# Performance work log

Hardware: AMD Instinct MI355X
Metric: run time of the kernel (lower is better)

## Reference

```python
import jax, jax.numpy as jnp
import numpy as np

B, D, T = 32, 6, 2048
FH, ENC, H, CONF, NC, K = 128, 128, 256, 64, 10, 5


def setup_inputs() -> dict:
    key = jax.random.key(0)
    ks = iter(jax.random.split(key, 40))
    n = lambda shape, s=0.05: jax.random.normal(next(ks), shape, dtype=jnp.float32) * s
    inp = {
        'M': jax.random.normal(next(ks), (B, D, T), dtype=jnp.float32),
        # causal conv frontend (4 dilated convs, kernel 5)
        'conv_w0': n((FH, D, K)), 'conv_b0': n((FH,)),
        'conv_w1': n((FH, FH, K)), 'conv_b1': n((FH,)),
        'conv_w2': n((FH, FH, K)), 'conv_b2': n((FH,)),
        'conv_w3': n((FH, FH, K)), 'conv_b3': n((FH,)),
        # encoder projection
        'enc_w': n((ENC, FH)), 'enc_b': n((ENC,)),
        # selective state space
        'A': n((H, H), 0.01), 'ip_w': n((H, ENC)), 'ip_b': n((H,)),
        'state_bias': jnp.zeros((H,), jnp.float32),
        'op_w': n((H, H)), 'op_b': n((H,)),
        # classifier head
        'cls_w1': n((256, H)), 'cls_b1': n((256,)),
        'cls_w2': n((NC, 256)), 'cls_b2': n((NC,)),
        # metanet: 2*D -> 64 -> 128 -> confound_dim
        'mn_w1': n((64, 2 * D)), 'mn_b1': n((64,)),
        'mn_w2': n((128, 64)), 'mn_b2': n((128,)),
        'mn_w3': n((CONF, 128)), 'mn_b3': n((CONF,)),
        # frontdoor: confound_dim -> 128 -> ssm_hidden
        'fd_w1': n((128, CONF)), 'fd_b1': n((128,)),
        'fd_w2': n((H, 128)), 'fd_b2': n((H,)),
    }
    return inp


def _causal_conv(x, w, b, d):
    # x: (B,C,T), w: (O,I,K). pad-left (K-1)*d == pad-both + trim-right in torch code
    y = jax.lax.conv_general_dilated(
        x, w, window_strides=(1,), padding=[((w.shape[2] - 1) * d, 0)],
        rhs_dilation=(d,), dimension_numbers=('NCH', 'OIH', 'NCH'))
    return jax.nn.relu(y + b[None, :, None])


def reference(M, conv_w0, conv_b0, conv_w1, conv_b1, conv_w2, conv_b2, conv_w3, conv_b3,
              enc_w, enc_b, A, ip_w, ip_b, state_bias, op_w, op_b,
              cls_w1, cls_b1, cls_w2, cls_b2,
              mn_w1, mn_b1, mn_w2, mn_b2, mn_w3, mn_b3,
              fd_w1, fd_b1, fd_w2, fd_b2):
    # frontend: 4 causal dilated convs with ReLU
    out = M
    for w, b, d in ((conv_w0, conv_b0, 1), (conv_w1, conv_b1, 2),
                    (conv_w2, conv_b2, 4), (conv_w3, conv_b3, 8)):
        out = _causal_conv(out, w, b, d)
    feat = jnp.einsum('bct,ec->bte', out, enc_w) + enc_b  # (B,T,ENC)
    # SSM: precompute input projection, then sequential scan over T
    u = jnp.einsum('bte,he->bth', feat, ip_w) + ip_b + state_bias  # (B,T,H)

    def step(h, ut):
        h = jax.nn.gelu(h @ A.T + ut, approximate=False)
        return h, h

    h0 = jnp.zeros((M.shape[0], A.shape[0]), M.dtype)
    _, hs = jax.lax.scan(step, h0, jnp.swapaxes(u, 0, 1))  # hs: (T,B,H)
    ssm_out = jnp.einsum('tbh,gh->btg', hs, op_w) + op_b  # (B,T,H)
    pooled = ssm_out.mean(axis=1)  # (B,H)
    logits = jax.nn.relu(pooled @ cls_w1.T + cls_b1) @ cls_w2.T + cls_b2
    # confounder summary: mean & unbiased std over time
    s = jnp.concatenate([M.mean(axis=2), jnp.std(M, axis=2, ddof=1)], axis=1)
    z = jax.nn.relu(s @ mn_w1.T + mn_b1)
    z = jax.nn.relu(z @ mn_w2.T + mn_b2)
    conf_hat = z @ mn_w3.T + mn_b3
    adj = jax.nn.relu(conf_hat @ fd_w1.T + fd_b1) @ fd_w2.T + fd_b2
    corrected = pooled - adj
    return (logits, pooled, corrected, conf_hat)
```

## Files before the change

kernel.cpp:

```cpp
#include <hip/hip_runtime.h>
#include <cmath>


typedef __bf16 bf16_t;
typedef bf16_t bf16x8 __attribute__((ext_vector_type(8)));
typedef bf16_t bf16x4 __attribute__((ext_vector_type(4)));
typedef float f32x4 __attribute__((ext_vector_type(4)));

__device__ __forceinline__ f32x4 mfma16(bf16x8 a, bf16x8 b, f32x4 c) {
  return __builtin_amdgcn_mfma_f32_16x16x32_bf16(a, b, c, 0, 0, 0);
}
__device__ __forceinline__ float gelu_fast(float x) {
  float x2 = x * x;
  float p = __builtin_fmaf(x2, -0.10295219f, -2.3022081278f);
  float e = __builtin_amdgcn_exp2f(x * p);
  return x * __builtin_amdgcn_rcpf(1.f + e);
}
__device__ __forceinline__ float bf2f(unsigned short us) {
  return __uint_as_float(((unsigned)us) << 16);
}

__global__ void k_repack(const float* __restrict__ w0, const float* __restrict__ w1,
                         const float* __restrict__ w2, const float* __restrict__ w3,
                         bf16_t* __restrict__ wb0, bf16_t* __restrict__ wb1,
                         bf16_t* __restrict__ wb2, bf16_t* __restrict__ wb3) {
  int idx = blockIdx.x * 256 + threadIdx.x;
  if (idx < 128 * 32) {
    int o = idx >> 5, k = idx & 31;
    float v = 0.f;
    if (k < 30) { int i = k / 5, kk = k - i * 5; v = w0[(o * 6 + i) * 5 + kk]; }
    wb0[idx] = (bf16_t)v;
    return;
  }
  int e = idx - 128 * 32;
  if (e < 3 * 5 * 128 * 128) {
    int layer = e / (5 * 128 * 128);
    int r = e - layer * (5 * 128 * 128);
    int ks = r / 16384;
    int o = (r >> 7) & 127;
    int i = r & 127;
    const float* w = layer == 0 ? w1 : layer == 1 ? w2 : w3;
    bf16_t* wb = layer == 0 ? wb1 : layer == 1 ? wb2 : wb3;
    wb[r] = (bf16_t)w[(o * 128 + i) * 5 + ks];
  }
}

__global__ void k_wce(const float* __restrict__ ip_w, const float* __restrict__ enc_w,
                      const float* __restrict__ enc_b, const float* __restrict__ ip_b,
                      const float* __restrict__ sbias, bf16_t* __restrict__ wce,
                      float* __restrict__ bce) {
  int h = blockIdx.x, c = threadIdx.x;
  float s = 0.f;
  for (int e = 0; e < 128; ++e) s += ip_w[h * 128 + e] * enc_w[e * 128 + c];
  wce[h * 128 + c] = (bf16_t)s;
  if (c == 0) {
    float bv = 0.f;
    for (int e = 0; e < 128; ++e) bv += ip_w[h * 128 + e] * enc_b[e];
    bce[h] = bv + ip_b[h] + sbias[h];
  }
}

__global__ __launch_bounds__(256) void k_conv0(const float* __restrict__ M,
                                               const bf16_t* __restrict__ wb0,
                                               const float* __restrict__ b0,
                                               bf16_t* __restrict__ out) {
  __shared__ float raw[6][136];
  __shared__ bf16_t Xe[128 * 40];
  const int tid = threadIdx.x;
  const int b = blockIdx.y, t0 = blockIdx.x * 128;
  for (int id = tid; id < 6 * 132; id += 256) {
    int i = id / 132, j = id - i * 132;
    int t = t0 - 4 + j;
    raw[i][j] = (t >= 0) ? M[((size_t)b * 6 + i) * 2048 + t] : 0.f;
  }
  __syncthreads();
  for (int id = tid; id < 128 * 32; id += 256) {
    int tl = id >> 5, k = id & 31;
    float v = 0.f;
    if (k < 30) { int i = k / 5, kk = k - i * 5; v = raw[i][tl + kk]; }
    Xe[tl * 40 + k] = (bf16_t)v;
  }
  __syncthreads();
  const int w = tid >> 6, lane = tid & 63, q = lane >> 4, l15 = lane & 15;
  const int k0 = q * 8;
  const f32x4 z4 = {0.f, 0.f, 0.f, 0.f};
  f32x4 acc[2][8];
#pragma unroll
  for (int mt = 0; mt < 2; ++mt)
#pragma unroll
    for (int nt = 0; nt < 8; ++nt) acc[mt][nt] = z4;
  bf16x8 af[2];
#pragma unroll
  for (int mt = 0; mt < 2; ++mt)
    af[mt] = *(const bf16x8*)&Xe[(w * 32 + mt * 16 + l15) * 40 + k0];
#pragma unroll
  for (int nt = 0; nt < 8; ++nt) {
    bf16x8 bf = *(const bf16x8*)&wb0[(nt * 16 + l15) * 32 + k0];
#pragma unroll
    for (int mt = 0; mt < 2; ++mt) acc[mt][nt] = mfma16(af[mt], bf, acc[mt][nt]);
  }
#pragma unroll
  for (int nt = 0; nt < 8; ++nt) {
    const int o = nt * 16 + l15;
    const float bias = b0[o];
#pragma unroll
    for (int mt = 0; mt < 2; ++mt) {
#pragma unroll
      for (int r = 0; r < 4; ++r) {
        int t = t0 + w * 32 + mt * 16 + q * 4 + r;
        float v = acc[mt][nt][r] + bias;
        out[((size_t)b * 2048 + t) * 128 + o] = (bf16_t)(v > 0.f ? v : 0.f);
      }
    }
  }
}

template <int DIL>
__global__ __launch_bounds__(256) void k_conv(const bf16_t* __restrict__ in,
                                              const bf16_t* __restrict__ wb,
                                              const float* __restrict__ bias,
                                              bf16_t* __restrict__ out) {
  __shared__ bf16_t Xs[160 * 136];
  const int tid = threadIdx.x;
  const int b = blockIdx.y, t0 = blockIdx.x * 128;
  const bf16_t* src = in + (size_t)b * 2048 * 128;
  for (int id = tid; id < 160 * 16; id += 256) {
    int r = id >> 4, ck = id & 15;
    int t = t0 + r - 32;
    int4 v = make_int4(0, 0, 0, 0);
    if (t >= 0) v = *(const int4*)(src + (size_t)t * 128 + ck * 8);
    *(int4*)&Xs[r * 136 + ck * 8] = v;
  }
  __syncthreads();
  const int w = tid >> 6, lane = tid & 63, q = lane >> 4, l15 = lane & 15;
  const f32x4 z4 = {0.f, 0.f, 0.f, 0.f};
  f32x4 acc[2][8];
#pragma unroll
  for (int mt = 0; mt < 2; ++mt)
#pragma unroll
    for (int nt = 0; nt < 8; ++nt) acc[mt][nt] = z4;
#pragma unroll
  for (int ks = 0; ks < 5; ++ks) {
    const int shift = (4 - ks) * DIL;
#pragma unroll
    for (int kt = 0; kt < 4; ++kt) {
      const int k0 = kt * 32 + q * 8;
      bf16x8 af[2];
#pragma unroll
      for (int mt = 0; mt < 2; ++mt)
        af[mt] = *(const bf16x8*)&Xs[(32 + w * 32 + mt * 16 + l15 - shift) * 136 + k0];
#pragma unroll
      for (int nt = 0; nt < 8; ++nt) {
        bf16x8 bf = *(const bf16x8*)&wb[((size_t)ks * 128 + nt * 16 + l15) * 128 + k0];
#pragma unroll
        for (int mt = 0; mt < 2; ++mt) acc[mt][nt] = mfma16(af[mt], bf, acc[mt][nt]);
      }
    }
  }
#pragma unroll
  for (int nt = 0; nt < 8; ++nt) {
    const int o = nt * 16 + l15;
    const float bv = bias[o];
#pragma unroll
    for (int mt = 0; mt < 2; ++mt) {
#pragma unroll
      for (int r = 0; r < 4; ++r) {
        int t = t0 + w * 32 + mt * 16 + q * 4 + r;
        float v = acc[mt][nt][r] + bv;
        out[((size_t)b * 2048 + t) * 128 + o] = (bf16_t)(v > 0.f ? v : 0.f);
      }
    }
  }
}

__global__ __launch_bounds__(256) void k_ugemm(const bf16_t* __restrict__ in,
                                               const bf16_t* __restrict__ wce,
                                               const float* __restrict__ bce,
                                               bf16_t* __restrict__ u) {
  __shared__ bf16_t Xs[128 * 136];
  const int tid = threadIdx.x;
  const int b = blockIdx.y, t0 = blockIdx.x * 128, hh = blockIdx.z;
  const bf16_t* src = in + (size_t)b * 2048 * 128;
  for (int id = tid; id < 128 * 16; id += 256) {
    int r = id >> 4, ck = id & 15;
    *(int4*)&Xs[r * 136 + ck * 8] = *(const int4*)(src + (size_t)(t0 + r) * 128 + ck * 8);
  }
  __syncthreads();
  const int w = tid >> 6, lane = tid & 63, q = lane >> 4, l15 = lane & 15;
  const f32x4 z4 = {0.f, 0.f, 0.f, 0.f};
  f32x4 acc[2][8];
#pragma unroll
  for (int mt = 0; mt < 2; ++mt)
#pragma unroll
    for (int nt = 0; nt < 8; ++nt) acc[mt][nt] = z4;
#pragma unroll
  for (int kt = 0; kt < 4; ++kt) {
    const int k0 = kt * 32 + q * 8;
    bf16x8 af[2];
#pragma unroll
    for (int mt = 0; mt < 2; ++mt)
      af[mt] = *(const bf16x8*)&Xs[(w * 32 + mt * 16 + l15) * 136 + k0];
#pragma unroll
    for (int nt = 0; nt < 8; ++nt) {
      bf16x8 bf = *(const bf16x8*)&wce[((size_t)hh * 128 + nt * 16 + l15) * 128 + k0];
#pragma unroll
      for (int mt = 0; mt < 2; ++mt) acc[mt][nt] = mfma16(af[mt], bf, acc[mt][nt]);
    }
  }
#pragma unroll
  for (int nt = 0; nt < 8; ++nt) {
    const int h = hh * 128 + nt * 16 + l15;
    const float bv = bce[h];
#pragma unroll
    for (int mt = 0; mt < 2; ++mt) {
#pragma unroll
      for (int r = 0; r < 4; ++r) {
        int t = t0 + w * 32 + mt * 16 + q * 4 + r;
        u[((size_t)b * 2048 + t) * 256 + h] = (bf16_t)(acc[mt][nt][r] + bv);
      }
    }
  }
}

__global__ __launch_bounds__(512, 2) void k_scan(const float* __restrict__ Am,
                                                 const bf16_t* __restrict__ u,
                                                 float* __restrict__ hbarOut) {
  __shared__ bf16_t Hs[2][16 * 256];
  const int b0 = blockIdx.x * 16;
  const int tid = threadIdx.x;
  const int wave = tid >> 6, lane = tid & 63, q = lane >> 4, l15 = lane & 15;

  bf16x8 afr[2][8];
#pragma unroll
  for (int ft = 0; ft < 2; ++ft) {
    const int f = wave * 32 + ft * 16 + l15;
#pragma unroll
    for (int kt = 0; kt < 8; ++kt) {
      const float* ap = Am + (size_t)f * 256 + kt * 32 + q * 8;
      f32x4 p0 = *(const f32x4*)ap;
      f32x4 p1 = *(const f32x4*)(ap + 4);
      bf16x8 v;
      v[0] = (bf16_t)p0[0]; v[1] = (bf16_t)p0[1]; v[2] = (bf16_t)p0[2]; v[3] = (bf16_t)p0[3];
      v[4] = (bf16_t)p1[0]; v[5] = (bf16_t)p1[1]; v[6] = (bf16_t)p1[2]; v[7] = (bf16_t)p1[3];
      afr[ft][kt] = v;
    }
  }
  for (int i = tid; i < 2 * 16 * 256 / 2; i += 512) ((int*)Hs)[i] = 0;

  const bf16_t* up = u + ((size_t)(b0 + l15) * 2048) * 256 + wave * 32 + q * 4;
  ushort4 uc[2], un[2];
#pragma unroll
  for (int ft = 0; ft < 2; ++ft) uc[ft] = *(const ushort4*)(up + ft * 16);
#pragma unroll
  for (int ft = 0; ft < 2; ++ft) un[ft] = *(const ushort4*)(up + 256 + ft * 16);

  float hbar[2][4];
#pragma unroll
  for (int ft = 0; ft < 2; ++ft)
#pragma unroll
    for (int r = 0; r < 4; ++r) hbar[ft][r] = 0.f;

  const int sw = l15 & 7;
  int rdoff[8];
#pragma unroll
  for (int kt = 0; kt < 8; ++kt) rdoff[kt] = l15 * 256 + (((kt * 4 + q) ^ sw) << 3);
  int wroff[2];
#pragma unroll
  for (int ft = 0; ft < 2; ++ft)
    wroff[ft] = l15 * 256 + (((wave * 4 + ft * 2 + (q >> 1)) ^ sw) << 3) + (q & 1) * 4;
  __syncthreads();

  int rd = 0;
  const f32x4 z4 = {0.f, 0.f, 0.f, 0.f};
#pragma unroll 2
  for (int t = 0; t < 2048; ++t) {
    bf16x8 hfr[8];
#pragma unroll
    for (int kt = 0; kt < 8; ++kt)
      hfr[kt] = *(const bf16x8*)&Hs[rd][rdoff[kt]];
    ushort4 u2[2];
    {
      size_t off = (size_t)(t + 2 <= 2047 ? t + 2 : 2047) * 256;
#pragma unroll
      for (int ft = 0; ft < 2; ++ft) u2[ft] = *(const ushort4*)(up + off + ft * 16);
    }
    f32x4 a0 = z4, a1 = z4;
#pragma unroll
    for (int kt = 0; kt < 8; ++kt) {
      a0 = mfma16(afr[0][kt], hfr[kt], a0);
      a1 = mfma16(afr[1][kt], hfr[kt], a1);
    }
    f32x4 acc01[2] = {a0, a1};
#pragma unroll
    for (int ft = 0; ft < 2; ++ft) {
      float g0 = gelu_fast(acc01[ft][0] + bf2f(uc[ft].x));
      float g1 = gelu_fast(acc01[ft][1] + bf2f(uc[ft].y));
      float g2 = gelu_fast(acc01[ft][2] + bf2f(uc[ft].z));
      float g3 = gelu_fast(acc01[ft][3] + bf2f(uc[ft].w));
      hbar[ft][0] += g0; hbar[ft][1] += g1; hbar[ft][2] += g2; hbar[ft][3] += g3;
      bf16x4 pk;
      pk[0] = (bf16_t)g0; pk[1] = (bf16_t)g1; pk[2] = (bf16_t)g2; pk[3] = (bf16_t)g3;
      *(bf16x4*)&Hs[rd ^ 1][wroff[ft]] = pk;
    }
    asm volatile("s_waitcnt lgkmcnt(0)\n\ts_barrier" ::: "memory");
#pragma unroll
    for (int ft = 0; ft < 2; ++ft) { uc[ft] = un[ft]; un[ft] = u2[ft]; }
    rd ^= 1;
  }
#pragma unroll
  for (int ft = 0; ft < 2; ++ft) {
    f32x4 vv;
#pragma unroll
    for (int r = 0; r < 4; ++r) vv[r] = hbar[ft][r] * (1.f / 2048.f);
    *(f32x4*)(hbarOut + (size_t)(b0 + l15) * 256 + wave * 32 + ft * 16 + q * 4) = vv;
  }
}

__global__ void k_meta1(const float* __restrict__ M, float* __restrict__ stats) {
  const int c = blockIdx.x, b = blockIdx.y, tid = threadIdx.x;
  const float* p = M + ((size_t)b * 6 + c) * 2048;
  float s = 0.f, ss = 0.f;
  for (int t = tid; t < 2048; t += 256) { float v = p[t]; s += v; ss += v * v; }
  for (int o = 32; o > 0; o >>= 1) { s += __shfl_down(s, o, 64); ss += __shfl_down(ss, o, 64); }
  __shared__ float as_[4], ass_[4];
  const int w = tid >> 6, lane = tid & 63;
  if (lane == 0) { as_[w] = s; ass_[w] = ss; }
  __syncthreads();
  if (tid == 0) {
    s = as_[0] + as_[1] + as_[2] + as_[3];
    ss = ass_[0] + ass_[1] + ass_[2] + ass_[3];
    float mean = s * (1.f / 2048.f);
    float var = (ss - 2048.f * mean * mean) * (1.f / 2047.f);
    if (var < 0.f) var = 0.f;
    stats[b * 12 + c] = mean;
    stats[b * 12 + 6 + c] = sqrtf(var);
  }
}

__global__ void k_meta2(const float* __restrict__ stats,
                        const float* __restrict__ w1, const float* __restrict__ b1,
                        const float* __restrict__ w2, const float* __restrict__ b2,
                        const float* __restrict__ w3, const float* __restrict__ b3,
                        const float* __restrict__ f1, const float* __restrict__ fb1,
                        const float* __restrict__ f2, const float* __restrict__ fb2,
                        float* __restrict__ out, float* __restrict__ adj) {
  const int b = blockIdx.x, tid = threadIdx.x;
  __shared__ float s[12], z1[64], z2[128], ch[64], a1[128];
  if (tid < 12) s[tid] = stats[b * 12 + tid];
  __syncthreads();
  if (tid < 64) {
    float v = b1[tid];
    for (int e = 0; e < 12; ++e) v += w1[tid * 12 + e] * s[e];
    z1[tid] = v > 0.f ? v : 0.f;
  }
  __syncthreads();
  if (tid < 128) {
    float v = b2[tid];
    for (int e = 0; e < 64; ++e) v += w2[tid * 64 + e] * z1[e];
    z2[tid] = v > 0.f ? v : 0.f;
  }
  __syncthreads();
  if (tid < 64) {
    float v = b3[tid];
    for (int e = 0; e < 128; ++e) v += w3[tid * 128 + e] * z2[e];
    ch[tid] = v;
    out[16704 + b * 64 + tid] = v;
  }
  __syncthreads();
  if (tid < 128) {
    float v = fb1[tid];
    for (int e = 0; e < 64; ++e) v += f1[tid * 64 + e] * ch[e];
    a1[tid] = v > 0.f ? v : 0.f;
  }
  __syncthreads();
  {
    float v = fb2[tid];
    for (int e = 0; e < 128; ++e) v += f2[tid * 128 + e] * a1[e];
    adj[b * 256 + tid] = v;
  }
}

__global__ void k_head(const float* __restrict__ hbar, const float* __restrict__ op_w,
                       const float* __restrict__ op_b, const float* __restrict__ cw1,
                       const float* __restrict__ cb1, const float* __restrict__ cw2,
                       const float* __restrict__ cb2, const float* __restrict__ adj,
                       float* __restrict__ out) {
  const int b = blockIdx.x, g = threadIdx.x;
  __shared__ float hs[256], ps[256], hid[256];
  hs[g] = hbar[b * 256 + g];
  __syncthreads();
  float v = op_b[g];
  for (int h = 0; h < 256; ++h) v += op_w[g * 256 + h] * hs[h];
  out[320 + b * 256 + g] = v;
  out[8512 + b * 256 + g] = v - adj[b * 256 + g];
  ps[g] = v;
  __syncthreads();
  float hv = cb1[g];
  for (int h = 0; h < 256; ++h) hv += cw1[g * 256 + h] * ps[h];
  hid[g] = hv > 0.f ? hv : 0.f;
  __syncthreads();
  if (g < 10) {
    float lv = cb2[g];
    for (int h = 0; h < 256; ++h) lv += cw2[g * 256 + h] * hid[h];
    out[b * 10 + g] = lv;
  }
}

extern "C" void kernel_launch(void* const* d_in, const int* in_sizes, int n_in,
                              void* d_out, int out_size, void* d_ws, size_t ws_size,
                              hipStream_t stream) {
  (void)in_sizes; (void)n_in; (void)out_size; (void)ws_size;
  const float* M    = (const float*)d_in[0];
  const float* w0   = (const float*)d_in[1];  const float* b0  = (const float*)d_in[2];
  const float* w1   = (const float*)d_in[3];  const float* b1  = (const float*)d_in[4];
  const float* w2   = (const float*)d_in[5];  const float* b2  = (const float*)d_in[6];
  const float* w3   = (const float*)d_in[7];  const float* b3  = (const float*)d_in[8];
  const float* encw = (const float*)d_in[9];  const float* encb = (const float*)d_in[10];
  const float* Am   = (const float*)d_in[11];
  const float* ipw  = (const float*)d_in[12]; const float* ipb = (const float*)d_in[13];
  const float* sb   = (const float*)d_in[14];
  const float* opw  = (const float*)d_in[15]; const float* opb = (const float*)d_in[16];
  const float* cw1  = (const float*)d_in[17]; const float* cb1 = (const float*)d_in[18];
  const float* cw2  = (const float*)d_in[19]; const float* cb2 = (const float*)d_in[20];
  const float* mw1  = (const float*)d_in[21]; const float* mb1 = (const float*)d_in[22];
  const float* mw2  = (const float*)d_in[23]; const float* mb2 = (const float*)d_in[24];
  const float* mw3  = (const float*)d_in[25]; const float* mb3 = (const float*)d_in[26];
  const float* fw1  = (const float*)d_in[27]; const float* fb1 = (const float*)d_in[28];
  const float* fw2  = (const float*)d_in[29]; const float* fb2 = (const float*)d_in[30];
  float* out = (float*)d_out;

  char* ws = (char*)d_ws;
  bf16_t* wb0  = (bf16_t*)(ws + 0);
  bf16_t* wb1  = (bf16_t*)(ws + 8192);
  bf16_t* wb2  = (bf16_t*)(ws + 172032);
  bf16_t* wb3  = (bf16_t*)(ws + 335872);
  bf16_t* wce  = (bf16_t*)(ws + 499712);
  float*  bce  = (float*) (ws + 565248);
  float*  hbar = (float*) (ws + 566272);
  float*  adj  = (float*) (ws + 599040);
  float*  stats= (float*) (ws + 631808);
  bf16_t* actA = (bf16_t*)(ws + 633856);
  bf16_t* actB = (bf16_t*)(ws + 17411072);
  bf16_t* u    = (bf16_t*)(ws + 34188288);

  k_repack<<<976, 256, 0, stream>>>(w0, w1, w2, w3, wb0, wb1, wb2, wb3);
  k_wce<<<256, 128, 0, stream>>>(ipw, encw, encb, ipb, sb, wce, bce);
  k_conv0<<<dim3(16, 32), 256, 0, stream>>>(M, wb0, b0, actA);
  k_conv<2><<<dim3(16, 32), 256, 0, stream>>>(actA, wb1, b1, actB);
  k_conv<4><<<dim3(16, 32), 256, 0, stream>>>(actB, wb2, b2, actA);
  k_conv<8><<<dim3(16, 32), 256, 0, stream>>>(actA, wb3, b3, actB);
  k_ugemm<<<dim3(16, 32, 2), 256, 0, stream>>>(actB, wce, bce, u);
  k_scan<<<2, 512, 0, stream>>>(Am, u, hbar);
  k_meta1<<<dim3(6, 32), 256, 0, stream>>>(M, stats);
  k_meta2<<<32, 256, 0, stream>>>(stats, mw1, mb1, mw2, mb2, mw3, mb3,
                                  fw1, fb1, fw2, fb2, out, adj);
  k_head<<<32, 256, 0, stream>>>(hbar, opw, opb, cw1, cb1, cw2, cb2, adj, out);
}
```

Before: 1.716 ms.

## Merge prep and meta kernels, restructure scan step with split MFMA chains

Folds the weight repack and encoder/input-projection precompute into one launch, and the metanet stats and MLP into one launch, cutting two kernel launches. The sequential scan loop is restructured. It manually unrolls by two with fixed LDS buffer offsets and splits the 8-deep MFMA accumulation into two independent chains. Odd waves iterate k-tiles in reverse order, and the hbar accumulation is deferred by one step to shorten the dependent path. The scan dominates runtime, so the latency-chain changes matter most. They cost more registers and add an extra vector add per step.

```diff
diff --git a/kernel.cpp b/kernel.cpp
--- a/kernel.cpp
+++ b/kernel.cpp
@@ -20,10 +20,27 @@
   return __uint_as_float(((unsigned)us) << 16);
 }
 
-__global__ void k_repack(const float* __restrict__ w0, const float* __restrict__ w1,
-                         const float* __restrict__ w2, const float* __restrict__ w3,
-                         bf16_t* __restrict__ wb0, bf16_t* __restrict__ wb1,
-                         bf16_t* __restrict__ wb2, bf16_t* __restrict__ wb3) {
+__global__ void k_prep(const float* __restrict__ w0, const float* __restrict__ w1,
+                       const float* __restrict__ w2, const float* __restrict__ w3,
+                       bf16_t* __restrict__ wb0, bf16_t* __restrict__ wb1,
+                       bf16_t* __restrict__ wb2, bf16_t* __restrict__ wb3,
+                       const float* __restrict__ ip_w, const float* __restrict__ enc_w,
+                       const float* __restrict__ enc_b, const float* __restrict__ ip_b,
+                       const float* __restrict__ sbias, bf16_t* __restrict__ wce,
+                       float* __restrict__ bce) {
+  if (blockIdx.x >= 976) {
+    const int hb = blockIdx.x - 976;
+    const int h = hb * 2 + (threadIdx.x >> 7), c = threadIdx.x & 127;
+    float s = 0.f;
+    for (int e = 0; e < 128; ++e) s += ip_w[h * 128 + e] * enc_w[e * 128 + c];
+    wce[h * 128 + c] = (bf16_t)s;
+    if (c == 0) {
+      float bv = 0.f;
+      for (int e = 0; e < 128; ++e) bv += ip_w[h * 128 + e] * enc_b[e];
+      bce[h] = bv + ip_b[h] + sbias[h];
+    }
+    return;
+  }
   int idx = blockIdx.x * 256 + threadIdx.x;
   if (idx < 128 * 32) {
     int o = idx >> 5, k = idx & 31;
@@ -42,21 +59,6 @@
     const float* w = layer == 0 ? w1 : layer == 1 ? w2 : w3;
     bf16_t* wb = layer == 0 ? wb1 : layer == 1 ? wb2 : wb3;
     wb[r] = (bf16_t)w[(o * 128 + i) * 5 + ks];
-  }
-}
-
-__global__ void k_wce(const float* __restrict__ ip_w, const float* __restrict__ enc_w,
-                      const float* __restrict__ enc_b, const float* __restrict__ ip_b,
-                      const float* __restrict__ sbias, bf16_t* __restrict__ wce,
-                      float* __restrict__ bce) {
-  int h = blockIdx.x, c = threadIdx.x;
-  float s = 0.f;
-  for (int e = 0; e < 128; ++e) s += ip_w[h * 128 + e] * enc_w[e * 128 + c];
-  wce[h * 128 + c] = (bf16_t)s;
-  if (c == 0) {
-    float bv = 0.f;
-    for (int e = 0; e < 128; ++e) bv += ip_w[h * 128 + e] * enc_b[e];
-    bce[h] = bv + ip_b[h] + sbias[h];
   }
 }
 
@@ -225,27 +227,39 @@
 __global__ __launch_bounds__(512, 2) void k_scan(const float* __restrict__ Am,
                                                  const bf16_t* __restrict__ u,
                                                  float* __restrict__ hbarOut) {
-  __shared__ bf16_t Hs[2][16 * 256];
+  __shared__ bf16_t HsF[2 * 16 * 256];
   const int b0 = blockIdx.x * 16;
   const int tid = threadIdx.x;
   const int wave = tid >> 6, lane = tid & 63, q = lane >> 4, l15 = lane & 15;
+  const int rev = wave & 1;
 
   bf16x8 afr[2][8];
-#pragma unroll
-  for (int ft = 0; ft < 2; ++ft) {
-    const int f = wave * 32 + ft * 16 + l15;
-#pragma unroll
-    for (int kt = 0; kt < 8; ++kt) {
+  int rdo0[8], rdo1[8];
+  const int sw = l15 & 7;
+#pragma unroll
+  for (int i = 0; i < 8; ++i) {
+    const int kt = rev ? 7 - i : i;
+#pragma unroll
+    for (int ft = 0; ft < 2; ++ft) {
+      const int f = wave * 32 + ft * 16 + l15;
       const float* ap = Am + (size_t)f * 256 + kt * 32 + q * 8;
       f32x4 p0 = *(const f32x4*)ap;
       f32x4 p1 = *(const f32x4*)(ap + 4);
       bf16x8 v;
       v[0] = (bf16_t)p0[0]; v[1] = (bf16_t)p0[1]; v[2] = (bf16_t)p0[2]; v[3] = (bf16_t)p0[3];
       v[4] = (bf16_t)p1[0]; v[5] = (bf16_t)p1[1]; v[6] = (bf16_t)p1[2]; v[7] = (bf16_t)p1[3];
-      afr[ft][kt] = v;
-    }
-  }
-  for (int i = tid; i < 2 * 16 * 256 / 2; i += 512) ((int*)Hs)[i] = 0;
+      afr[ft][i] = v;
+    }
+    rdo0[i] = l15 * 256 + (((kt * 4 + q) ^ sw) << 3);
+    rdo1[i] = 4096 + rdo0[i];
+  }
+  int wro0[2], wro1[2];
+#pragma unroll
+  for (int ft = 0; ft < 2; ++ft) {
+    wro0[ft] = l15 * 256 + (((wave * 4 + ft * 2 + (q >> 1)) ^ sw) << 3) + (q & 1) * 4;
+    wro1[ft] = 4096 + wro0[ft];
+  }
+  for (int i = tid; i < 2 * 16 * 256 / 2; i += 512) ((int*)HsF)[i] = 0;
 
   const bf16_t* up = u + ((size_t)(b0 + l15) * 2048) * 256 + wave * 32 + q * 4;
   ushort4 uc[2], un[2];
@@ -254,100 +268,106 @@
 #pragma unroll
   for (int ft = 0; ft < 2; ++ft) un[ft] = *(const ushort4*)(up + 256 + ft * 16);
 
-  float hbar[2][4];
-#pragma unroll
-  for (int ft = 0; ft < 2; ++ft)
-#pragma unroll
-    for (int r = 0; r < 4; ++r) hbar[ft][r] = 0.f;
-
-  const int sw = l15 & 7;
-  int rdoff[8];
-#pragma unroll
-  for (int kt = 0; kt < 8; ++kt) rdoff[kt] = l15 * 256 + (((kt * 4 + q) ^ sw) << 3);
-  int wroff[2];
-#pragma unroll
-  for (int ft = 0; ft < 2; ++ft)
-    wroff[ft] = l15 * 256 + (((wave * 4 + ft * 2 + (q >> 1)) ^ sw) << 3) + (q & 1) * 4;
-  __syncthreads();
-
-  int rd = 0;
+  f32x4 hbar0 = {0.f, 0.f, 0.f, 0.f}, hbar1 = {0.f, 0.f, 0.f, 0.f};
+  f32x4 gprev0 = {0.f, 0.f, 0.f, 0.f}, gprev1 = {0.f, 0.f, 0.f, 0.f};
   const f32x4 z4 = {0.f, 0.f, 0.f, 0.f};
-#pragma unroll 2
-  for (int t = 0; t < 2048; ++t) {
+  __syncthreads();
+
+  auto step = [&](const int* rdo, const int* wro, int t) __attribute__((always_inline)) {
     bf16x8 hfr[8];
 #pragma unroll
-    for (int kt = 0; kt < 8; ++kt)
-      hfr[kt] = *(const bf16x8*)&Hs[rd][rdoff[kt]];
+    for (int i = 0; i < 8; ++i) hfr[i] = *(const bf16x8*)&HsF[rdo[i]];
     ushort4 u2[2];
     {
       size_t off = (size_t)(t + 2 <= 2047 ? t + 2 : 2047) * 256;
-#pragma unroll
-      for (int ft = 0; ft < 2; ++ft) u2[ft] = *(const ushort4*)(up + off + ft * 16);
-    }
-    f32x4 a0 = z4, a1 = z4;
-#pragma unroll
-    for (int kt = 0; kt < 8; ++kt) {
-      a0 = mfma16(afr[0][kt], hfr[kt], a0);
-      a1 = mfma16(afr[1][kt], hfr[kt], a1);
-    }
-    f32x4 acc01[2] = {a0, a1};
-#pragma unroll
-    for (int ft = 0; ft < 2; ++ft) {
-      float g0 = gelu_fast(acc01[ft][0] + bf2f(uc[ft].x));
-      float g1 = gelu_fast(acc01[ft][1] + bf2f(uc[ft].y));
-      float g2 = gelu_fast(acc01[ft][2] + bf2f(uc[ft].z));
-      float g3 = gelu_fast(acc01[ft][3] + bf2f(uc[ft].w));
-      hbar[ft][0] += g0; hbar[ft][1] += g1; hbar[ft][2] += g2; hbar[ft][3] += g3;
+      u2[0] = *(const ushort4*)(up + off);
+      u2[1] = *(const ushort4*)(up + off + 16);
+    }
+    hbar0 += gprev0;
+    hbar1 += gprev1;
+    f32x4 c0a = z4, c0b = z4, c1a = z4, c1b = z4;
+#pragma unroll
+    for (int i = 0; i < 4; ++i) {
+      c0a = mfma16(afr[0][i], hfr[i], c0a);
+      c1a = mfma16(afr[1][i], hfr[i], c1a);
+    }
+#pragma unroll
+    for (int i = 4; i < 8; ++i) {
+      c0b = mfma16(afr[0][i], hfr[i], c0b);
+      c1b = mfma16(afr[1][i], hfr[i], c1b);
+    }
+    f32x4 y0 = c0a + c0b;
+    {
+      float g0 = gelu_fast(y0[0] + bf2f(uc[0].x));
+      float g1 = gelu_fast(y0[1] + bf2f(uc[0].y));
+      float g2 = gelu_fast(y0[2] + bf2f(uc[0].z));
+      float g3 = gelu_fast(y0[3] + bf2f(uc[0].w));
       bf16x4 pk;
       pk[0] = (bf16_t)g0; pk[1] = (bf16_t)g1; pk[2] = (bf16_t)g2; pk[3] = (bf16_t)g3;
-      *(bf16x4*)&Hs[rd ^ 1][wroff[ft]] = pk;
+      *(bf16x4*)&HsF[wro[0]] = pk;
+      gprev0[0] = g0; gprev0[1] = g1; gprev0[2] = g2; gprev0[3] = g3;
+    }
+    f32x4 y1 = c1a + c1b;
+    {
+      float g0 = gelu_fast(y1[0] + bf2f(uc[1].x));
+      float g1 = gelu_fast(y1[1] + bf2f(uc[1].y));
+      float g2 = gelu_fast(y1[2] + bf2f(uc[1].z));
+      float g3 = gelu_fast(y1[3] + bf2f(uc[1].w));
+      bf16x4 pk;
+      pk[0] = (bf16_t)g0; pk[1] = (bf16_t)g1; pk[2] = (bf16_t)g2; pk[3] = (bf16_t)g3;
+      *(bf16x4*)&HsF[wro[1]] = pk;
+      gprev1[0] = g0; gprev1[1] = g1; gprev1[2] = g2; gprev1[3] = g3;
     }
     asm volatile("s_waitcnt lgkmcnt(0)\n\ts_barrier" ::: "memory");
-#pragma unroll
-    for (int ft = 0; ft < 2; ++ft) { uc[ft] = un[ft]; un[ft] = u2[ft]; }
-    rd ^= 1;
-  }
-#pragma unroll
-  for (int ft = 0; ft < 2; ++ft) {
-    f32x4 vv;
-#pragma unroll
-    for (int r = 0; r < 4; ++r) vv[r] = hbar[ft][r] * (1.f / 2048.f);
-    *(f32x4*)(hbarOut + (size_t)(b0 + l15) * 256 + wave * 32 + ft * 16 + q * 4) = vv;
-  }
-}
-
-__global__ void k_meta1(const float* __restrict__ M, float* __restrict__ stats) {
-  const int c = blockIdx.x, b = blockIdx.y, tid = threadIdx.x;
-  const float* p = M + ((size_t)b * 6 + c) * 2048;
-  float s = 0.f, ss = 0.f;
-  for (int t = tid; t < 2048; t += 256) { float v = p[t]; s += v; ss += v * v; }
-  for (int o = 32; o > 0; o >>= 1) { s += __shfl_down(s, o, 64); ss += __shfl_down(ss, o, 64); }
-  __shared__ float as_[4], ass_[4];
+    uc[0] = un[0]; uc[1] = un[1];
+    un[0] = u2[0]; un[1] = u2[1];
+  };
+
+  for (int t = 0; t < 2048; t += 2) {
+    step(rdo0, wro1, t);
+    step(rdo1, wro0, t + 1);
+  }
+  hbar0 += gprev0;
+  hbar1 += gprev1;
+
+  {
+    f32x4 v0, v1;
+#pragma unroll
+    for (int r = 0; r < 4; ++r) { v0[r] = hbar0[r] * (1.f / 2048.f); v1[r] = hbar1[r] * (1.f / 2048.f); }
+    float* dst = hbarOut + (size_t)(b0 + l15) * 256 + wave * 32 + q * 4;
+    *(f32x4*)(dst) = v0;
+    *(f32x4*)(dst + 16) = v1;
+  }
+}
+
+__global__ void k_meta(const float* __restrict__ M,
+                       const float* __restrict__ w1, const float* __restrict__ b1,
+                       const float* __restrict__ w2, const float* __restrict__ b2,
+                       const float* __restrict__ w3, const float* __restrict__ b3,
+                       const float* __restrict__ f1, const float* __restrict__ fb1,
+                       const float* __restrict__ f2, const float* __restrict__ fb2,
+                       float* __restrict__ out, float* __restrict__ adj) {
+  const int b = blockIdx.x, tid = threadIdx.x;
   const int w = tid >> 6, lane = tid & 63;
-  if (lane == 0) { as_[w] = s; ass_[w] = ss; }
-  __syncthreads();
-  if (tid == 0) {
-    s = as_[0] + as_[1] + as_[2] + as_[3];
-    ss = ass_[0] + ass_[1] + ass_[2] + ass_[3];
-    float mean = s * (1.f / 2048.f);
-    float var = (ss - 2048.f * mean * mean) * (1.f / 2047.f);
-    if (var < 0.f) var = 0.f;
-    stats[b * 12 + c] = mean;
-    stats[b * 12 + 6 + c] = sqrtf(var);
-  }
-}
-
-__global__ void k_meta2(const float* __restrict__ stats,
-                        const float* __restrict__ w1, const float* __restrict__ b1,
-                        const float* __restrict__ w2, const float* __restrict__ b2,
-                        const float* __restrict__ w3, const float* __restrict__ b3,
-                        const float* __restrict__ f1, const float* __restrict__ fb1,
-                        const float* __restrict__ f2, const float* __restrict__ fb2,
-                        float* __restrict__ out, float* __restrict__ adj) {
-  const int b = blockIdx.x, tid = threadIdx.x;
-  __shared__ float s[12], z1[64], z2[128], ch[64], a1[128];
-  if (tid < 12) s[tid] = stats[b * 12 + tid];
-  __syncthreads();
+  __shared__ float s[12], red[8], z1[64], z2[128], ch[64], a1[128];
+  for (int c = 0; c < 6; ++c) {
+    const float* p = M + ((size_t)b * 6 + c) * 2048;
+    float sum = 0.f, ss = 0.f;
+    for (int t = tid; t < 2048; t += 256) { float v = p[t]; sum += v; ss += v * v; }
+    for (int o = 32; o > 0; o >>= 1) { sum += __shfl_down(sum, o, 64); ss += __shfl_down(ss, o, 64); }
+    if (lane == 0) { red[w * 2] = sum; red[w * 2 + 1] = ss; }
+    __syncthreads();
+    if (tid == 0) {
+      sum = red[0] + red[2] + red[4] + red[6];
+      ss = red[1] + red[3] + red[5] + red[7];
+      float mean = sum * (1.f / 2048.f);
+      float var = (ss - 2048.f * mean * mean) * (1.f / 2047.f);
+      if (var < 0.f) var = 0.f;
+      s[c] = mean;
+      s[6 + c] = sqrtf(var);
+    }
+    __syncthreads();
+  }
   if (tid < 64) {
     float v = b1[tid];
     for (int e = 0; e < 12; ++e) v += w1[tid * 12 + e] * s[e];
@@ -438,21 +458,19 @@
   float*  bce  = (float*) (ws + 565248);
   float*  hbar = (float*) (ws + 566272);
   float*  adj  = (float*) (ws + 599040);
-  float*  stats= (float*) (ws + 631808);
   bf16_t* actA = (bf16_t*)(ws + 633856);
   bf16_t* actB = (bf16_t*)(ws + 17411072);
   bf16_t* u    = (bf16_t*)(ws + 34188288);
 
-  k_repack<<<976, 256, 0, stream>>>(w0, w1, w2, w3, wb0, wb1, wb2, wb3);
-  k_wce<<<256, 128, 0, stream>>>(ipw, encw, encb, ipb, sb, wce, bce);
+  k_prep<<<1104, 256, 0, stream>>>(w0, w1, w2, w3, wb0, wb1, wb2, wb3,
+                                   ipw, encw, encb, ipb, sb, wce, bce);
   k_conv0<<<dim3(16, 32), 256, 0, stream>>>(M, wb0, b0, actA);
   k_conv<2><<<dim3(16, 32), 256, 0, stream>>>(actA, wb1, b1, actB);
   k_conv<4><<<dim3(16, 32), 256, 0, stream>>>(actB, wb2, b2, actA);
   k_conv<8><<<dim3(16, 32), 256, 0, stream>>>(actA, wb3, b3, actB);
   k_ugemm<<<dim3(16, 32, 2), 256, 0, stream>>>(actB, wce, bce, u);
   k_scan<<<2, 512, 0, stream>>>(Am, u, hbar);
-  k_meta1<<<dim3(6, 32), 256, 0, stream>>>(M, stats);
-  k_meta2<<<32, 256, 0, stream>>>(stats, mw1, mb1, mw2, mb2, mw3, mb3,
-                                  fw1, fb1, fw2, fb2, out, adj);
+  k_meta<<<32, 256, 0, stream>>>(M, mw1, mb1, mw2, mb2, mw3, mb3,
+                                 fw1, fb1, fw2, fb2, out, adj);
   k_head<<<32, 256, 0, stream>>>(hbar, opw, opb, cw1, cb1, cw2, cb2, adj, out);
 }
```

Result: slower. 1.765 ms (+2.8%).
